# Performance work log

Measured on AMD Instinct MI355X. Metric: run time of the kernel, lower is better.

Reference implementation:

```python
import jax, jax.numpy as jnp
import numpy as np

N_EMBD = 1024
N_HEAD = 16


def setup_inputs() -> dict:
    key = jax.random.key(0)
    ks = jax.random.split(key, 5)
    B, T, C = 2, 2048, N_EMBD
    x = jax.random.normal(ks[0], (B, T, C), dtype=jnp.float32)
    # parameters (stored as (in, out); forward uses x @ W + b, equivalent to torch Linear)
    s1 = 1.0 / np.sqrt(C)
    W_attn = jax.random.normal(ks[1], (C, 3 * C), dtype=jnp.float32) * s1
    b_attn = jnp.zeros((3 * C,), dtype=jnp.float32)
    W_proj = jax.random.normal(ks[2], (C, C), dtype=jnp.float32) * s1
    b_proj = jnp.zeros((C,), dtype=jnp.float32)
    return {"x": x, "W_attn": W_attn, "b_attn": b_attn, "W_proj": W_proj, "b_proj": b_proj}


def reference(x, W_attn, b_attn, W_proj, b_proj):
    B, T, C = x.shape
    H = N_HEAD
    D = C // H  # head dim
    qkv = x @ W_attn + b_attn                       # [B, T, 3C]
    q, k, v = jnp.split(qkv, 3, axis=-1)
    # [B, H, T, D]
    q = q.reshape(B, T, H, D).transpose(0, 2, 1, 3)
    k = k.reshape(B, T, H, D).transpose(0, 2, 1, 3)
    v = v.reshape(B, T, H, D).transpose(0, 2, 1, 3)
    scale = 1.0 / jnp.sqrt(jnp.asarray(D, dtype=q.dtype))
    wei = jnp.einsum("bhqd,bhkd->bhqk", q, k) * scale  # [B, H, T, T]
    causal = jnp.tril(jnp.ones((T, T), dtype=bool))
    wei = jnp.where(causal[None, None, :, :], wei, -jnp.inf)
    wei = jax.nn.softmax(wei, axis=-1)
    y = jnp.einsum("bhqk,bhkd->bhqd", wei, v)          # [B, H, T, D]
    y = y.transpose(0, 2, 1, 3).reshape(B, T, C)
    return y @ W_proj + b_proj
```

## Files before the change

kernel.cpp:

```cpp
#include <hip/hip_runtime.h>
#include <hip/hip_bf16.h>

typedef __attribute__((ext_vector_type(8))) short short8;
typedef __attribute__((ext_vector_type(4))) float floatx4;
typedef __attribute__((ext_vector_type(4))) unsigned int uintx4;
#define BF16 __hip_bfloat16

__device__ __forceinline__ unsigned short f2bf(float f) {
  unsigned int u = __builtin_bit_cast(unsigned int, f);
  unsigned int r = (u + 0x7FFFu + ((u >> 16) & 1u)) >> 16;
  return (unsigned short)r;
}

__device__ __forceinline__ unsigned int cvt_pk_bf16(float lo, float hi) {
  unsigned int r;
  asm("v_cvt_pk_bf16_f32 %0, %1, %2" : "=v"(r) : "v"(lo), "v"(hi));
  return r;
}

__device__ __forceinline__ void gload_lds16(const void* g, void* l) {
  __builtin_amdgcn_global_load_lds(
      (const __attribute__((address_space(1))) unsigned int*)g,
      (__attribute__((address_space(3))) unsigned int*)l, 16, 0, 0);
}

__global__ __launch_bounds__(256)
void prep_fused(const float* __restrict__ x, unsigned short* __restrict__ xb,
                const float* __restrict__ Wa, unsigned short* __restrict__ wta,
                const float* __restrict__ Wp, unsigned short* __restrict__ wtp) {
  __shared__ float tile[64][65];
  const int blk = blockIdx.x;
  const int tid = threadIdx.x;

  if (blk < 2048) {
    int i = (blk * 256 + tid) * 8;
    float4 a = *(const float4*)(x + i);
    float4 b = *(const float4*)(x + i + 4);
    short8 v;
    v[0] = (short)f2bf(a.x); v[1] = (short)f2bf(a.y);
    v[2] = (short)f2bf(a.z); v[3] = (short)f2bf(a.w);
    v[4] = (short)f2bf(b.x); v[5] = (short)f2bf(b.y);
    v[6] = (short)f2bf(b.z); v[7] = (short)f2bf(b.w);
    *(short8*)(xb + i) = v;
    return;
  }

  const float* in;
  unsigned short* out;
  int K = 1024, N, bb;
  if (blk < 2816) { in = Wa; out = wta; N = 3072; bb = blk - 2048; }
  else            { in = Wp; out = wtp; N = 1024; bb = blk - 2816; }
  const int nb = N >> 6;
  const int tn = bb % nb, tk = bb / nb;
  const int n0 = tn << 6, k0 = tk << 6;
#pragma unroll
  for (int c = 0; c < 4; ++c) {
    int t = tid + c * 256;
    int r = t >> 4, col = (t & 15) << 2;
    float4 v = *(const float4*)(in + (size_t)(k0 + r) * N + n0 + col);
    tile[r][col] = v.x; tile[r][col + 1] = v.y;
    tile[r][col + 2] = v.z; tile[r][col + 3] = v.w;
  }
  __syncthreads();
#pragma unroll
  for (int c = 0; c < 2; ++c) {
    int t = tid + c * 256;
    int r = t >> 3, col = (t & 7) << 3;
    short8 v;
#pragma unroll
    for (int j = 0; j < 8; ++j) v[j] = (short)f2bf(tile[col + j][r]);
    *(short8*)(out + (size_t)(n0 + r) * K + k0 + col) = v;
  }
}

__global__ __launch_bounds__(256, 2)
void gemm_qkv(const BF16* __restrict__ A, const BF16* __restrict__ Bt,
              const float* __restrict__ bias, BF16* __restrict__ out,
              int M, int N, int K) {
  const int tid = threadIdx.x;
  const int w = tid >> 6, l = tid & 63;
  const int lr = l & 15, lg = l >> 4;
  const int nbx = N >> 7;
  const int bm = blockIdx.x / nbx, bn = blockIdx.x % nbx;
  const int row0 = bm << 7, col0 = bn << 7;
  const int wr = (w >> 1) << 6, wc = (w & 1) << 6;

  __shared__ __align__(16) BF16 ldsA[128 * 64];
  __shared__ __align__(16) BF16 ldsB[128 * 64];

  floatx4 acc[4][4] = {};
  const int swzl = (lr & 7) << 3;

  for (int k0 = 0; k0 < K; k0 += 64) {
#pragma unroll
    for (int c = 0; c < 4; ++c) {
      int t = w * 64 + l + c * 256;
      int ar = t >> 3;
      int ch = (t & 7) ^ (ar & 7);
      gload_lds16(A + (size_t)(row0 + ar) * K + k0 + (ch << 3),
                  ldsA + w * 512 + c * 2048);
      gload_lds16(Bt + (size_t)(col0 + ar) * K + k0 + (ch << 3),
                  ldsB + w * 512 + c * 2048);
    }
    __syncthreads();
#pragma unroll
    for (int kk = 0; kk < 64; kk += 32) {
      short8 af[4], bf[4];
#pragma unroll
      for (int m = 0; m < 4; ++m)
        af[m] = *(const short8*)(ldsA + (wr + m * 16 + lr) * 64 + ((kk + lg * 8) ^ swzl));
#pragma unroll
      for (int n = 0; n < 4; ++n)
        bf[n] = *(const short8*)(ldsB + (wc + n * 16 + lr) * 64 + ((kk + lg * 8) ^ swzl));
#pragma unroll
      for (int m = 0; m < 4; ++m)
#pragma unroll
        for (int n = 0; n < 4; ++n)
          acc[m][n] = __builtin_amdgcn_mfma_f32_16x16x32_bf16(af[m], bf[n], acc[m][n], 0, 0, 0);
    }
    __syncthreads();
  }

#pragma unroll
  for (int m = 0; m < 4; ++m)
#pragma unroll
    for (int n = 0; n < 4; ++n)
#pragma unroll
      for (int j = 0; j < 4; ++j) {
        int row = row0 + wr + m * 16 + lg * 4 + j;
        int col = col0 + wc + n * 16 + lr;
        float v = acc[m][n][j] + bias[col];
        int s = col >> 10, cc = col & 1023;
        int hh = cc >> 6, dd = cc & 63;
        int bb = row >> 11, tt = row & 2047;
        size_t addr;
        if (s == 2)
          addr = (size_t)8388608 + (((size_t)bb * 16 + hh) * 64 + dd) * 2048 + tt;
        else
          addr = (size_t)s * 4194304 + (((size_t)bb * 16 + hh) * 2048 + tt) * 64 + dd;
        out[addr] = __float2bfloat16(v);
      }
}

__global__ __launch_bounds__(256, 4)
void gemm_proj(const BF16* __restrict__ A, const BF16* __restrict__ Bt,
               const float* __restrict__ bias, float* __restrict__ out,
               int M, int N, int K) {
  const int tid = threadIdx.x;
  const int w = tid >> 6, l = tid & 63;
  const int lr = l & 15, lg = l >> 4;
  const int bm = blockIdx.x >> 3, bn = blockIdx.x & 7;
  const int row0 = bm << 6, col0 = bn << 7;
  const int wr = (w >> 1) << 5, wc = (w & 1) << 6;

  __shared__ __align__(16) BF16 ldsA[64 * 64];
  __shared__ __align__(16) BF16 ldsB[128 * 64];

  floatx4 acc[2][4] = {};
  const int swzl = (lr & 7) << 3;

  for (int k0 = 0; k0 < K; k0 += 64) {
#pragma unroll
    for (int c = 0; c < 2; ++c) {
      int t = w * 64 + l + c * 256;
      int ar = t >> 3;
      int ch = (t & 7) ^ (ar & 7);
      gload_lds16(A + (size_t)(row0 + ar) * K + k0 + (ch << 3),
                  ldsA + w * 512 + c * 2048);
    }
#pragma unroll
    for (int c = 0; c < 4; ++c) {
      int t = w * 64 + l + c * 256;
      int br = t >> 3;
      int ch = (t & 7) ^ (br & 7);
      gload_lds16(Bt + (size_t)(col0 + br) * K + k0 + (ch << 3),
                  ldsB + w * 512 + c * 2048);
    }
    __syncthreads();
#pragma unroll
    for (int kk = 0; kk < 64; kk += 32) {
      short8 af[2], bf[4];
#pragma unroll
      for (int m = 0; m < 2; ++m)
        af[m] = *(const short8*)(ldsA + (wr + m * 16 + lr) * 64 + ((kk + lg * 8) ^ swzl));
#pragma unroll
      for (int n = 0; n < 4; ++n)
        bf[n] = *(const short8*)(ldsB + (wc + n * 16 + lr) * 64 + ((kk + lg * 8) ^ swzl));
#pragma unroll
      for (int m = 0; m < 2; ++m)
#pragma unroll
        for (int n = 0; n < 4; ++n)
          acc[m][n] = __builtin_amdgcn_mfma_f32_16x16x32_bf16(af[m], bf[n], acc[m][n], 0, 0, 0);
    }
    __syncthreads();
  }

#pragma unroll
  for (int m = 0; m < 2; ++m)
#pragma unroll
    for (int n = 0; n < 4; ++n)
#pragma unroll
      for (int j = 0; j < 4; ++j) {
        int row = row0 + wr + m * 16 + lg * 4 + j;
        int col = col0 + wc + n * 16 + lr;
        out[(size_t)row * N + col] = acc[m][n][j] + bias[col];
      }
}

__global__ __launch_bounds__(256, 5)
void flash_attn(const BF16* __restrict__ qkv, BF16* __restrict__ y) {
  const int T = 2048;
  const int i = blockIdx.x;
  const int xcd = i & 7, s = i >> 3;
  const int par = (s ^ (s >> 5)) & 1;
  const int rnk = ((s >> 5) << 4) | ((s & 31) >> 1);
  const int bh = xcd * 4 + (rnk & 3);
  const int hq = rnk >> 2;
  const int qt = par ? hq : (31 - hq);
  const int b = bh >> 4, h = bh & 15;
  const int q0 = qt << 6;
  const int tid = threadIdx.x, w = tid >> 6, l = tid & 63;
  const int lr = l & 15, lg = l >> 4;

  const BF16* Q  = qkv + (size_t)bh * T * 64;
  const BF16* Kp = qkv + 4194304 + (size_t)bh * T * 64;
  const BF16* Vt = qkv + 8388608 + (size_t)bh * 64 * T;

  __shared__ __align__(16) BF16 ldsK[2][4096];
  __shared__ __align__(16) BF16 ldsV[2][4096];

  const float C1 = 0.18033688011112042f;
  const float C2 = 17.312340490667562f;
  const int swzl = (lr & 7) << 3;
  const int nt = qt + 1;

  short8 qf[2];
#pragma unroll
  for (int c = 0; c < 2; ++c)
    qf[c] = *(const short8*)(Q + (size_t)(q0 + w * 16 + lr) * 64 + c * 32 + lg * 8);

  floatx4 acc_o[4] = {};
  floatx4 lsum4 = {0.f, 0.f, 0.f, 0.f};

  const int t0 = w * 64 + l, t1 = t0 + 256;
  const int r0 = t0 >> 3, ch0 = (t0 & 7) ^ (r0 & 7);
  const int r1 = t1 >> 3, ch1 = (t1 & 7) ^ (r1 & 7);
  const BF16* kg0 = Kp + ((size_t)r0 << 6) + ch0 * 8;
  const BF16* kg1 = Kp + ((size_t)r1 << 6) + ch1 * 8;
  const BF16* vg0 = Vt + (size_t)r0 * T + ch0 * 8;
  const BF16* vg1 = Vt + (size_t)r1 * T + ch1 * 8;

#define STAGE2(BUF)                                           \
  {                                                           \
    gload_lds16(kg0, &ldsK[BUF][w * 512]);                    \
    gload_lds16(vg0, &ldsV[BUF][w * 512]);                    \
    gload_lds16(kg1, &ldsK[BUF][w * 512 + 2048]);             \
    gload_lds16(vg1, &ldsV[BUF][w * 512 + 2048]);             \
    kg0 += 4096; kg1 += 4096; vg0 += 64; vg1 += 64;           \
  }

#define TILE(IT, MASKED)                                                      \
  {                                                                           \
    const int cur_ = (IT) & 1;                                                \
    if ((IT) + 1 < nt) {                                                      \
      STAGE2(cur_ ^ 1);                                                       \
      asm volatile("s_waitcnt vmcnt(4)" ::: "memory");    \
    } else {                                                                  \
      asm volatile("s_waitcnt vmcnt(0)" ::: "memory");                        \
    }                                                                         \
    __builtin_amdgcn_s_barrier();                                             \
    floatx4 accs[4] = {};                                                     \
    __builtin_amdgcn_s_setprio(1);                                            \
    _Pragma("unroll")                                                         \
    for (int c = 0; c < 2; ++c)                                               \
      _Pragma("unroll")                                                       \
      for (int n4 = 0; n4 < 4; ++n4) {                                        \
        short8 kf = *(const short8*)(&ldsK[cur_][(n4 * 16 + lr) * 64 +        \
                                                ((c * 32 + lg * 8) ^ swzl)]); \
        accs[n4] = __builtin_amdgcn_mfma_f32_16x16x32_bf16(kf, qf[c], accs[n4], 0, 0, 0); \
      }                                                                       \
    __builtin_amdgcn_s_setprio(0);                                            \
    _Pragma("unroll")                                                         \
    for (int n4 = 0; n4 < 4; ++n4)                                            \
      _Pragma("unroll")                                                       \
      for (int j = 0; j < 4; ++j) {                                           \
        float p = exp2f(fmaf(accs[n4][j], C1, -C2));                          \
        if (MASKED && (n4 * 16 + lg * 4 + j > w * 16 + lr)) p = 0.f;          \
        lsum4[j] += p;                                                        \
        accs[n4][j] = p;                                                      \
      }                                                                       \
    __builtin_amdgcn_s_setprio(1);                                            \
    _Pragma("unroll")                                                         \
    for (int c = 0; c < 2; ++c) {                                             \
      unsigned int a0 = cvt_pk_bf16(accs[2 * c][0], accs[2 * c][1]);          \
      unsigned int b0 = cvt_pk_bf16(accs[2 * c + 1][0], accs[2 * c + 1][1]);  \
      unsigned int a1 = cvt_pk_bf16(accs[2 * c][2], accs[2 * c][3]);          \
      unsigned int b1 = cvt_pk_bf16(accs[2 * c + 1][2], accs[2 * c + 1][3]);  \
      asm("v_permlane32_swap_b32 %0, %1" : "+v"(a0), "+v"(b0));               \
      asm("v_permlane32_swap_b32 %0, %1" : "+v"(a1), "+v"(b1));               \
      asm("v_permlane16_swap_b32 %0, %1" : "+v"(a0), "+v"(b0));               \
      asm("v_permlane16_swap_b32 %0, %1" : "+v"(a1), "+v"(b1));               \
      uintx4 pw; pw[0] = a0; pw[1] = a1; pw[2] = b0; pw[3] = b1;              \
      short8 pf = __builtin_bit_cast(short8, pw);                             \
      _Pragma("unroll")                                                       \
      for (int n4 = 0; n4 < 4; ++n4) {                                        \
        short8 vf = *(const short8*)(&ldsV[cur_][(n4 * 16 + lr) * 64 +        \
                                                ((c * 32 + lg * 8) ^ swzl)]); \
        acc_o[n4] = __builtin_amdgcn_mfma_f32_16x16x32_bf16(pf, vf, acc_o[n4], 0, 0, 0); \
      }                                                                       \
    }                                                                         \
    __builtin_amdgcn_s_setprio(0);                                            \
    __builtin_amdgcn_s_barrier();                                             \
  }

  STAGE2(0);
  for (int it = 0; it < nt - 1; ++it) TILE(it, false);
  TILE(nt - 1, true);
#undef TILE
#undef STAGE2

  float lsum = (lsum4[0] + lsum4[1]) + (lsum4[2] + lsum4[3]);
  lsum += __shfl_xor(lsum, 16, 64);
  lsum += __shfl_xor(lsum, 32, 64);
  float inv_own = 1.0f / lsum;
  float inv[4];
#pragma unroll
  for (int j = 0; j < 4; ++j) inv[j] = __shfl(inv_own, lg * 4 + j, 64);
#pragma unroll
  for (int n4 = 0; n4 < 4; ++n4)
#pragma unroll
    for (int j = 0; j < 4; ++j) {
      int qr = q0 + w * 16 + lg * 4 + j;
      int dd = n4 * 16 + lr;
      y[((size_t)b * 2048 + qr) * 1024 + h * 64 + dd] =
          __float2bfloat16(acc_o[n4][j] * inv[j]);
    }
}

extern "C" void kernel_launch(void* const* d_in, const int* in_sizes, int n_in,
                              void* d_out, int out_size, void* d_ws, size_t ws_size,
                              hipStream_t stream) {
  const float* x      = (const float*)d_in[0];
  const float* W_attn = (const float*)d_in[1];
  const float* b_attn = (const float*)d_in[2];
  const float* W_proj = (const float*)d_in[3];
  const float* b_proj = (const float*)d_in[4];
  float* out = (float*)d_out;
  BF16* ws  = (BF16*)d_ws;

  BF16* xb      = ws;
  BF16* wt_attn = xb + 4194304;
  BF16* wt_proj = wt_attn + 3145728;
  BF16* qkv     = wt_proj + 1048576;
  BF16* y       = qkv + 12582912;

  hipLaunchKernelGGL(prep_fused, dim3(3072), dim3(256), 0, stream,
                     x, (unsigned short*)xb,
                     W_attn, (unsigned short*)wt_attn,
                     W_proj, (unsigned short*)wt_proj);
  hipLaunchKernelGGL(gemm_qkv, dim3(32 * 24), dim3(256), 0, stream,
                     xb, wt_attn, b_attn, qkv, 4096, 3072, 1024);
  hipLaunchKernelGGL(flash_attn, dim3(1024), dim3(256), 0, stream, qkv, y);
  hipLaunchKernelGGL(gemm_proj, dim3(512), dim3(256), 0, stream,
                     y, wt_proj, b_proj, out, 4096, 1024, 1024);
}
```

Baseline: 103.1 us.

## Pair complementary causal query tiles per flash-attention block to share K/V loads

Each attention block now processes two query tiles, qt=31-pr and qt=pr, which share the same K/V stream. The block loads K/V once for both tiles and stops computing the short tile after its diagonal. This balances causal work across blocks and halves K/V traffic for the overlapping range. Grid size halves to 512 and launch bounds drop to 2 waves per SIMD, trading occupancy and register pressure for more MFMA work per LDS load.

```diff
diff --git a/kernel.cpp b/kernel.cpp
--- a/kernel.cpp
+++ b/kernel.cpp
@@ -207,18 +207,16 @@
       }
 }
 
-__global__ __launch_bounds__(256, 5)
+__global__ __launch_bounds__(256, 2)
 void flash_attn(const BF16* __restrict__ qkv, BF16* __restrict__ y) {
   const int T = 2048;
-  const int i = blockIdx.x;
-  const int xcd = i & 7, s = i >> 3;
-  const int par = (s ^ (s >> 5)) & 1;
-  const int rnk = ((s >> 5) << 4) | ((s & 31) >> 1);
-  const int bh = xcd * 4 + (rnk & 3);
-  const int hq = rnk >> 2;
-  const int qt = par ? hq : (31 - hq);
+  const int bid = blockIdx.x;
+  const int bh = (bid & 7) * 4 + ((bid >> 3) & 3);
+  const int pr = bid >> 5;
   const int b = bh >> 4, h = bh & 15;
-  const int q0 = qt << 6;
+  const int qtA = 31 - pr, qtB = pr;
+  const int q0A = qtA << 6, q0B = qtB << 6;
+  const int nt = qtA + 1;
   const int tid = threadIdx.x, w = tid >> 6, l = tid & 63;
   const int lr = l & 15, lg = l >> 4;
 
@@ -232,15 +230,16 @@
   const float C1 = 0.18033688011112042f;
   const float C2 = 17.312340490667562f;
   const int swzl = (lr & 7) << 3;
-  const int nt = qt + 1;
-
-  short8 qf[2];
-#pragma unroll
-  for (int c = 0; c < 2; ++c)
-    qf[c] = *(const short8*)(Q + (size_t)(q0 + w * 16 + lr) * 64 + c * 32 + lg * 8);
-
-  floatx4 acc_o[4] = {};
-  floatx4 lsum4 = {0.f, 0.f, 0.f, 0.f};
+
+  short8 qfA[2], qfB[2];
+#pragma unroll
+  for (int c = 0; c < 2; ++c) {
+    qfA[c] = *(const short8*)(Q + (size_t)(q0A + w * 16 + lr) * 64 + c * 32 + lg * 8);
+    qfB[c] = *(const short8*)(Q + (size_t)(q0B + w * 16 + lr) * 64 + c * 32 + lg * 8);
+  }
+
+  floatx4 acc_oA[4] = {}, acc_oB[4] = {};
+  floatx4 lsA4 = {0.f, 0.f, 0.f, 0.f}, lsB4 = {0.f, 0.f, 0.f, 0.f};
 
   const int t0 = w * 64 + l, t1 = t0 + 256;
   const int r0 = t0 >> 3, ch0 = (t0 & 7) ^ (r0 & 7);
@@ -259,17 +258,18 @@
     kg0 += 4096; kg1 += 4096; vg0 += 64; vg1 += 64;           \
   }
 
-#define TILE(IT, MASKED)                                                      \
+#define TILE(IT, DOB, MASKA, MASKB)                                           \
   {                                                                           \
     const int cur_ = (IT) & 1;                                                \
     if ((IT) + 1 < nt) {                                                      \
       STAGE2(cur_ ^ 1);                                                       \
-      asm volatile("s_waitcnt vmcnt(4)" ::: "memory");    \
+      asm volatile("s_waitcnt vmcnt(4)" ::: "memory");                        \
     } else {                                                                  \
       asm volatile("s_waitcnt vmcnt(0)" ::: "memory");                        \
     }                                                                         \
     __builtin_amdgcn_s_barrier();                                             \
-    floatx4 accs[4] = {};                                                     \
+    floatx4 accsA[4] = {};                                                    \
+    floatx4 accsB[4] = {};                                                    \
     __builtin_amdgcn_s_setprio(1);                                            \
     _Pragma("unroll")                                                         \
     for (int c = 0; c < 2; ++c)                                               \
@@ -277,36 +277,59 @@
       for (int n4 = 0; n4 < 4; ++n4) {                                        \
         short8 kf = *(const short8*)(&ldsK[cur_][(n4 * 16 + lr) * 64 +        \
                                                 ((c * 32 + lg * 8) ^ swzl)]); \
-        accs[n4] = __builtin_amdgcn_mfma_f32_16x16x32_bf16(kf, qf[c], accs[n4], 0, 0, 0); \
+        accsA[n4] = __builtin_amdgcn_mfma_f32_16x16x32_bf16(kf, qfA[c], accsA[n4], 0, 0, 0); \
+        if (DOB)                                                              \
+          accsB[n4] = __builtin_amdgcn_mfma_f32_16x16x32_bf16(kf, qfB[c], accsB[n4], 0, 0, 0); \
       }                                                                       \
     __builtin_amdgcn_s_setprio(0);                                            \
     _Pragma("unroll")                                                         \
     for (int n4 = 0; n4 < 4; ++n4)                                            \
       _Pragma("unroll")                                                       \
       for (int j = 0; j < 4; ++j) {                                           \
-        float p = exp2f(fmaf(accs[n4][j], C1, -C2));                          \
-        if (MASKED && (n4 * 16 + lg * 4 + j > w * 16 + lr)) p = 0.f;          \
-        lsum4[j] += p;                                                        \
-        accs[n4][j] = p;                                                      \
+        float pA = exp2f(fmaf(accsA[n4][j], C1, -C2));                        \
+        if (MASKA && (n4 * 16 + lg * 4 + j > w * 16 + lr)) pA = 0.f;          \
+        lsA4[j] += pA;                                                        \
+        accsA[n4][j] = pA;                                                    \
+        if (DOB) {                                                            \
+          float pB = exp2f(fmaf(accsB[n4][j], C1, -C2));                      \
+          if (MASKB && (n4 * 16 + lg * 4 + j > w * 16 + lr)) pB = 0.f;        \
+          lsB4[j] += pB;                                                      \
+          accsB[n4][j] = pB;                                                  \
+        }                                                                     \
       }                                                                       \
     __builtin_amdgcn_s_setprio(1);                                            \
     _Pragma("unroll")                                                         \
     for (int c = 0; c < 2; ++c) {                                             \
-      unsigned int a0 = cvt_pk_bf16(accs[2 * c][0], accs[2 * c][1]);          \
-      unsigned int b0 = cvt_pk_bf16(accs[2 * c + 1][0], accs[2 * c + 1][1]);  \
-      unsigned int a1 = cvt_pk_bf16(accs[2 * c][2], accs[2 * c][3]);          \
-      unsigned int b1 = cvt_pk_bf16(accs[2 * c + 1][2], accs[2 * c + 1][3]);  \
+      unsigned int a0 = cvt_pk_bf16(accsA[2 * c][0], accsA[2 * c][1]);        \
+      unsigned int b0 = cvt_pk_bf16(accsA[2 * c + 1][0], accsA[2 * c + 1][1]);\
+      unsigned int a1 = cvt_pk_bf16(accsA[2 * c][2], accsA[2 * c][3]);        \
+      unsigned int b1 = cvt_pk_bf16(accsA[2 * c + 1][2], accsA[2 * c + 1][3]);\
       asm("v_permlane32_swap_b32 %0, %1" : "+v"(a0), "+v"(b0));               \
       asm("v_permlane32_swap_b32 %0, %1" : "+v"(a1), "+v"(b1));               \
       asm("v_permlane16_swap_b32 %0, %1" : "+v"(a0), "+v"(b0));               \
       asm("v_permlane16_swap_b32 %0, %1" : "+v"(a1), "+v"(b1));               \
-      uintx4 pw; pw[0] = a0; pw[1] = a1; pw[2] = b0; pw[3] = b1;              \
-      short8 pf = __builtin_bit_cast(short8, pw);                             \
+      uintx4 pwA; pwA[0] = a0; pwA[1] = a1; pwA[2] = b0; pwA[3] = b1;         \
+      short8 pfA = __builtin_bit_cast(short8, pwA);                           \
+      short8 pfB;                                                             \
+      if (DOB) {                                                              \
+        unsigned int c0 = cvt_pk_bf16(accsB[2 * c][0], accsB[2 * c][1]);      \
+        unsigned int d0 = cvt_pk_bf16(accsB[2 * c + 1][0], accsB[2 * c + 1][1]); \
+        unsigned int c1 = cvt_pk_bf16(accsB[2 * c][2], accsB[2 * c][3]);      \
+        unsigned int d1 = cvt_pk_bf16(accsB[2 * c + 1][2], accsB[2 * c + 1][3]); \
+        asm("v_permlane32_swap_b32 %0, %1" : "+v"(c0), "+v"(d0));             \
+        asm("v_permlane32_swap_b32 %0, %1" : "+v"(c1), "+v"(d1));             \
+        asm("v_permlane16_swap_b32 %0, %1" : "+v"(c0), "+v"(d0));             \
+        asm("v_permlane16_swap_b32 %0, %1" : "+v"(c1), "+v"(d1));             \
+        uintx4 pwB; pwB[0] = c0; pwB[1] = c1; pwB[2] = d0; pwB[3] = d1;       \
+        pfB = __builtin_bit_cast(short8, pwB);                                \
+      }                                                                       \
       _Pragma("unroll")                                                       \
       for (int n4 = 0; n4 < 4; ++n4) {                                        \
         short8 vf = *(const short8*)(&ldsV[cur_][(n4 * 16 + lr) * 64 +        \
                                                 ((c * 32 + lg * 8) ^ swzl)]); \
-        acc_o[n4] = __builtin_amdgcn_mfma_f32_16x16x32_bf16(pf, vf, acc_o[n4], 0, 0, 0); \
+        acc_oA[n4] = __builtin_amdgcn_mfma_f32_16x16x32_bf16(pfA, vf, acc_oA[n4], 0, 0, 0); \
+        if (DOB)                                                              \
+          acc_oB[n4] = __builtin_amdgcn_mfma_f32_16x16x32_bf16(pfB, vf, acc_oB[n4], 0, 0, 0); \
       }                                                                       \
     }                                                                         \
     __builtin_amdgcn_s_setprio(0);                                            \
@@ -314,26 +337,37 @@
   }
 
   STAGE2(0);
-  for (int it = 0; it < nt - 1; ++it) TILE(it, false);
-  TILE(nt - 1, true);
+  int it = 0;
+  for (; it < pr; ++it) TILE(it, true, false, false);
+  TILE(pr, true, false, true);
+  ++it;
+  for (; it < nt - 1; ++it) TILE(it, false, false, false);
+  TILE(nt - 1, false, true, false);
 #undef TILE
 #undef STAGE2
 
-  float lsum = (lsum4[0] + lsum4[1]) + (lsum4[2] + lsum4[3]);
-  lsum += __shfl_xor(lsum, 16, 64);
-  lsum += __shfl_xor(lsum, 32, 64);
-  float inv_own = 1.0f / lsum;
-  float inv[4];
-#pragma unroll
-  for (int j = 0; j < 4; ++j) inv[j] = __shfl(inv_own, lg * 4 + j, 64);
+  float lsA = (lsA4[0] + lsA4[1]) + (lsA4[2] + lsA4[3]);
+  float lsB = (lsB4[0] + lsB4[1]) + (lsB4[2] + lsB4[3]);
+  lsA += __shfl_xor(lsA, 16, 64); lsA += __shfl_xor(lsA, 32, 64);
+  lsB += __shfl_xor(lsB, 16, 64); lsB += __shfl_xor(lsB, 32, 64);
+  float invA_own = 1.0f / lsA, invB_own = 1.0f / lsB;
+  float invA[4], invB[4];
+#pragma unroll
+  for (int j = 0; j < 4; ++j) {
+    invA[j] = __shfl(invA_own, lg * 4 + j, 64);
+    invB[j] = __shfl(invB_own, lg * 4 + j, 64);
+  }
 #pragma unroll
   for (int n4 = 0; n4 < 4; ++n4)
 #pragma unroll
     for (int j = 0; j < 4; ++j) {
-      int qr = q0 + w * 16 + lg * 4 + j;
+      int rA = q0A + w * 16 + lg * 4 + j;
+      int rB = q0B + w * 16 + lg * 4 + j;
       int dd = n4 * 16 + lr;
-      y[((size_t)b * 2048 + qr) * 1024 + h * 64 + dd] =
-          __float2bfloat16(acc_o[n4][j] * inv[j]);
+      y[((size_t)b * 2048 + rA) * 1024 + h * 64 + dd] =
+          __float2bfloat16(acc_oA[n4][j] * invA[j]);
+      y[((size_t)b * 2048 + rB) * 1024 + h * 64 + dd] =
+          __float2bfloat16(acc_oB[n4][j] * invB[j]);
     }
 }
 
@@ -360,7 +394,7 @@
                      W_proj, (unsigned short*)wt_proj);
   hipLaunchKernelGGL(gemm_qkv, dim3(32 * 24), dim3(256), 0, stream,
                      xb, wt_attn, b_attn, qkv, 4096, 3072, 1024);
-  hipLaunchKernelGGL(flash_attn, dim3(1024), dim3(256), 0, stream, qkv, y);
+  hipLaunchKernelGGL(flash_attn, dim3(512), dim3(256), 0, stream, qkv, y);
   hipLaunchKernelGGL(gemm_proj, dim3(512), dim3(256), 0, stream,
                      y, wt_proj, b_proj, out, 4096, 1024, 1024);
 }
```

Result: no change. 103.1 us (-0.0%).

## Stage 128-key K/V tiles per barrier pair in flash attention

Applied to the files above, without the earlier changes.

The flash attention loop now loads 128 keys of K and V per stage instead of 64, using double-buffered 32KB LDS buffers, and processes them as two 64-key sub-tiles between each barrier pair. This halves the number of barrier and wait points per query tile and issues larger async global-to-LDS batches. In exchange, LDS use quadruples, so occupancy is lowered (launch bounds go from 5 to 2 blocks). The final odd tile may load keys beyond the causal range, which are never consumed.

```diff
diff --git a/kernel.cpp b/kernel.cpp
--- a/kernel.cpp
+++ b/kernel.cpp
@@ -207,7 +207,7 @@
       }
 }
 
-__global__ __launch_bounds__(256, 5)
+__global__ __launch_bounds__(256, 2)
 void flash_attn(const BF16* __restrict__ qkv, BF16* __restrict__ y) {
   const int T = 2048;
   const int i = blockIdx.x;
@@ -226,13 +226,14 @@
   const BF16* Kp = qkv + 4194304 + (size_t)bh * T * 64;
   const BF16* Vt = qkv + 8388608 + (size_t)bh * 64 * T;
 
-  __shared__ __align__(16) BF16 ldsK[2][4096];
-  __shared__ __align__(16) BF16 ldsV[2][4096];
+  __shared__ __align__(16) BF16 ldsK[2][8192];
+  __shared__ __align__(16) BF16 ldsV[2][8192];
 
   const float C1 = 0.18033688011112042f;
   const float C2 = 17.312340490667562f;
   const int swzl = (lr & 7) << 3;
   const int nt = qt + 1;
+  const int iters = (nt + 1) >> 1;
 
   short8 qf[2];
 #pragma unroll
@@ -242,53 +243,55 @@
   floatx4 acc_o[4] = {};
   floatx4 lsum4 = {0.f, 0.f, 0.f, 0.f};
 
-  const int t0 = w * 64 + l, t1 = t0 + 256;
-  const int r0 = t0 >> 3, ch0 = (t0 & 7) ^ (r0 & 7);
-  const int r1 = t1 >> 3, ch1 = (t1 & 7) ^ (r1 & 7);
-  const BF16* kg0 = Kp + ((size_t)r0 << 6) + ch0 * 8;
-  const BF16* kg1 = Kp + ((size_t)r1 << 6) + ch1 * 8;
-  const BF16* vg0 = Vt + (size_t)r0 * T + ch0 * 8;
-  const BF16* vg1 = Vt + (size_t)r1 * T + ch1 * 8;
-
-#define STAGE2(BUF)                                           \
-  {                                                           \
-    gload_lds16(kg0, &ldsK[BUF][w * 512]);                    \
-    gload_lds16(vg0, &ldsV[BUF][w * 512]);                    \
-    gload_lds16(kg1, &ldsK[BUF][w * 512 + 2048]);             \
-    gload_lds16(vg1, &ldsV[BUF][w * 512 + 2048]);             \
-    kg0 += 4096; kg1 += 4096; vg0 += 64; vg1 += 64;           \
-  }
-
-#define TILE(IT, MASKED)                                                      \
+  const BF16* kg[4];
+  const BF16* vg[4];
+#pragma unroll
+  for (int c = 0; c < 4; ++c) {
+    int t = tid + c * 256;
+    int rk = t >> 3, chk = (t & 7) ^ (rk & 7);
+    kg[c] = Kp + ((size_t)rk << 6) + chk * 8;
+    int rv = t >> 4, chv = (t & 15) ^ (rv & 7);
+    vg[c] = Vt + (size_t)rv * T + chv * 8;
+  }
+
+#define FBARRIER asm volatile("s_barrier" ::: "memory")
+#define STAGE(BUF)                                                 \
+  { _Pragma("unroll")                                              \
+    for (int c = 0; c < 4; ++c) {                                  \
+      gload_lds16(kg[c], &ldsK[BUF][tid * 8 + c * 2048]);          \
+      gload_lds16(vg[c], &ldsV[BUF][tid * 8 + c * 2048]);          \
+      kg[c] += 8192; vg[c] += 128;                                 \
+    } }
+
+#define SUB(SB, DG)                                                           \
   {                                                                           \
-    const int cur_ = (IT) & 1;                                                \
-    if ((IT) + 1 < nt) {                                                      \
-      STAGE2(cur_ ^ 1);                                                       \
-      asm volatile("s_waitcnt vmcnt(4)" ::: "memory");    \
-    } else {                                                                  \
-      asm volatile("s_waitcnt vmcnt(0)" ::: "memory");                        \
-    }                                                                         \
-    __builtin_amdgcn_s_barrier();                                             \
     floatx4 accs[4] = {};                                                     \
     __builtin_amdgcn_s_setprio(1);                                            \
     _Pragma("unroll")                                                         \
     for (int c = 0; c < 2; ++c)                                               \
       _Pragma("unroll")                                                       \
       for (int n4 = 0; n4 < 4; ++n4) {                                        \
-        short8 kf = *(const short8*)(&ldsK[cur_][(n4 * 16 + lr) * 64 +        \
-                                                ((c * 32 + lg * 8) ^ swzl)]); \
+        short8 kf = *(const short8*)(&ldsK[cur][(SB * 64 + n4 * 16 + lr) * 64 \
+                                      + ((c * 32 + lg * 8) ^ swzl)]);         \
         accs[n4] = __builtin_amdgcn_mfma_f32_16x16x32_bf16(kf, qf[c], accs[n4], 0, 0, 0); \
       }                                                                       \
     __builtin_amdgcn_s_setprio(0);                                            \
     _Pragma("unroll")                                                         \
     for (int n4 = 0; n4 < 4; ++n4)                                            \
       _Pragma("unroll")                                                       \
-      for (int j = 0; j < 4; ++j) {                                           \
-        float p = exp2f(fmaf(accs[n4][j], C1, -C2));                          \
-        if (MASKED && (n4 * 16 + lg * 4 + j > w * 16 + lr)) p = 0.f;          \
-        lsum4[j] += p;                                                        \
-        accs[n4][j] = p;                                                      \
-      }                                                                       \
+      for (int j = 0; j < 4; ++j)                                             \
+        accs[n4][j] = exp2f(fmaf(accs[n4][j], C1, -C2));                      \
+    if (DG) {                                                                 \
+      _Pragma("unroll")                                                       \
+      for (int n4 = 0; n4 < 4; ++n4)                                          \
+        _Pragma("unroll")                                                     \
+        for (int j = 0; j < 4; ++j)                                           \
+          if (n4 * 16 + lg * 4 + j > w * 16 + lr) accs[n4][j] = 0.f;          \
+    }                                                                         \
+    _Pragma("unroll")                                                         \
+    for (int n4 = 0; n4 < 4; ++n4)                                            \
+      _Pragma("unroll")                                                       \
+      for (int j = 0; j < 4; ++j) lsum4[j] += accs[n4][j];                    \
     __builtin_amdgcn_s_setprio(1);                                            \
     _Pragma("unroll")                                                         \
     for (int c = 0; c < 2; ++c) {                                             \
@@ -304,20 +307,32 @@
       short8 pf = __builtin_bit_cast(short8, pw);                             \
       _Pragma("unroll")                                                       \
       for (int n4 = 0; n4 < 4; ++n4) {                                        \
-        short8 vf = *(const short8*)(&ldsV[cur_][(n4 * 16 + lr) * 64 +        \
-                                                ((c * 32 + lg * 8) ^ swzl)]); \
+        short8 vf = *(const short8*)(&ldsV[cur][(n4 * 16 + lr) * 128 +        \
+                            ((SB * 64 + c * 32 + lg * 8) ^ swzl)]);           \
         acc_o[n4] = __builtin_amdgcn_mfma_f32_16x16x32_bf16(pf, vf, acc_o[n4], 0, 0, 0); \
       }                                                                       \
     }                                                                         \
     __builtin_amdgcn_s_setprio(0);                                            \
-    __builtin_amdgcn_s_barrier();                                             \
-  }
-
-  STAGE2(0);
-  for (int it = 0; it < nt - 1; ++it) TILE(it, false);
-  TILE(nt - 1, true);
-#undef TILE
-#undef STAGE2
+  }
+
+  STAGE(0);
+  for (int it = 0; it < iters; ++it) {
+    const int cur = it & 1;
+    if (it + 1 < iters) {
+      STAGE(cur ^ 1);
+      asm volatile("s_waitcnt vmcnt(8)" ::: "memory");
+    } else {
+      asm volatile("s_waitcnt vmcnt(0)" ::: "memory");
+    }
+    FBARRIER;
+    const int jt0 = 2 * it;
+    SUB(0, jt0 == qt);
+    if (jt0 + 1 < nt) SUB(1, jt0 + 1 == qt);
+    FBARRIER;
+  }
+#undef SUB
+#undef STAGE
+#undef FBARRIER
 
   float lsum = (lsum4[0] + lsum4[1]) + (lsum4[2] + lsum4[3]);
   lsum += __shfl_xor(lsum, 16, 64);
```

After: 109.4 us. +6.1%, slower.
